# Optimization experiments

Hardware: AMD Instinct MI355X
Metric: run time of the kernel (lower is better)

The kernel has to match this reference:

```python
import jax, jax.numpy as jnp
import numpy as np
import math

N, D, H, DK, DV, FF = 2048, 1024, 16, 64, 64, 4096
EPS = 1e-5


def setup_inputs() -> dict:
    key = jax.random.key(0)
    ks = jax.random.split(key, 10)
    s = 0.02  # scaled init for numerical stability (original uses torch.randn)
    return {
        "x": jax.random.normal(ks[0], (N, D), dtype=jnp.float32),
        # per-head projections stacked: [H, D, DK/DV]
        "w_q": jax.random.normal(ks[1], (H, D, DK), dtype=jnp.float32) * s,
        "w_k": jax.random.normal(ks[2], (H, D, DK), dtype=jnp.float32) * s,
        "w_v": jax.random.normal(ks[3], (H, D, DV), dtype=jnp.float32) * s,
        "w_o": jax.random.normal(ks[4], (H * DV, D), dtype=jnp.float32) * s,
        "ln1_g": jnp.ones((D,), jnp.float32),
        "ln1_b": jnp.zeros((D,), jnp.float32),
        # FFN: Linear stored as [in, out] so y = x @ w + b
        "w1": jax.random.normal(ks[5], (D, FF), dtype=jnp.float32) * s,
        "b1": jnp.zeros((FF,), jnp.float32),
        "w2": jax.random.normal(ks[6], (FF, D), dtype=jnp.float32) * s,
        "b2": jnp.zeros((D,), jnp.float32),
        "ln2_g": jnp.ones((D,), jnp.float32),
        "ln2_b": jnp.zeros((D,), jnp.float32),
    }


def _layernorm(x, g, b):
    mu = jnp.mean(x, axis=-1, keepdims=True)
    var = jnp.mean(jnp.square(x - mu), axis=-1, keepdims=True)
    return (x - mu) * jax.lax.rsqrt(var + EPS) * g + b


def reference(x, w_q, w_k, w_v, w_o, ln1_g, ln1_b, w1, b1, w2, b2, ln2_g, ln2_b):
    n = x.shape[0]
    # multi-head causal self-attention (heads batched instead of Python loop)
    q = jnp.einsum('nd,hdk->hnk', x, w_q)  # [H,N,DK]
    k = jnp.einsum('nd,hdk->hnk', x, w_k)
    v = jnp.einsum('nd,hdv->hnv', x, w_v)
    scores = jnp.einsum('hnk,hmk->hnm', q, k) / math.sqrt(DK)  # [H,N,N]
    causal = jnp.tril(jnp.ones((n, n), dtype=bool))
    scores = jnp.where(causal, scores, -jnp.inf)
    probs = jax.nn.softmax(scores, axis=-1)
    attn = jnp.einsum('hnm,hmv->hnv', probs, v)  # [H,N,DV]
    concat = jnp.transpose(attn, (1, 0, 2)).reshape(n, H * DV)  # head-order concat
    mha = concat @ w_o  # [N,D]
    # residual + LN, FFN (note: ReLU after BOTH linears, as in the source)
    h = _layernorm(x + mha, ln1_g, ln1_b)
    ff = jax.nn.relu(jax.nn.relu(h @ w1 + b1) @ w2 + b2)
    return _layernorm(h + ff, ln2_g, ln2_b)
```

## Files before the change

### kernel.cpp

```cpp
#include <hip/hip_runtime.h>
#include <math.h>


#define NTOK   2048
#define DMODEL 1024
#define NHEAD  16
#define DHEAD  64
#define DFF    4096
#define LNEPS  1e-5f

typedef unsigned int   u32;
typedef unsigned short u16;
typedef __attribute__((ext_vector_type(8))) short short8;
typedef __attribute__((ext_vector_type(4))) float f32x4;

__device__ __forceinline__ u16 f2b(float f) {
    u32 b = __float_as_uint(f);
    b += 0x7FFFu + ((b >> 16) & 1u);
    return (u16)(b >> 16);
}

#define AS1(p) ((const __attribute__((address_space(1))) u32*)(p))
#define AS3(p) ((__attribute__((address_space(3))) u32*)(p))

template<int RELU, int BIAS, int RESID, int OUT_BF16, int SPLITK>
__global__ __launch_bounds__(256) void mfma_gemm(
    const u16* __restrict__ A, int lda,
    const u16* __restrict__ Bt, int ldbt,
    void* __restrict__ Cp, int ldc, int Kc,
    const float* __restrict__ bias,
    const float* __restrict__ resid, int ldr,
    size_t pstride)
{
    __shared__ u16 As[2][128 * 32];
    __shared__ u16 Bs[2][128 * 32];

    const int tid = threadIdx.x;
    const int l = tid & 63, w = tid >> 6;
    const int row0 = blockIdx.y * 128, col0 = blockIdx.x * 128;
    const int kbase = (SPLITK > 1) ? blockIdx.z * Kc : 0;

    f32x4 acc[4][4];
    #pragma unroll
    for (int m = 0; m < 4; ++m)
        #pragma unroll
        for (int n = 0; n < 4; ++n)
            acc[m][n] = (f32x4){0.f, 0.f, 0.f, 0.f};

    const int srow = w * 32 + (l >> 2);
    const int skk  = (l & 3) * 8;
    const u16* Ag = A  + (size_t)(row0 + srow) * lda  + kbase + skk;
    const u16* Bg = Bt + (size_t)(col0 + srow) * ldbt + kbase + skk;

    const int fr  = l & 15;
    const int fk  = (l >> 4) * 8;
    const int ar0 = (w >> 1) * 64;
    const int bc0 = (w & 1) * 64;

    auto STAGE = [&](int buf, int k0) {
        char* AsB = (char*)&As[buf][0] + w * 2048;
        char* BsB = (char*)&Bs[buf][0] + w * 2048;
        __builtin_amdgcn_global_load_lds(AS1(Ag + k0),                     AS3(AsB),        16, 0, 0);
        __builtin_amdgcn_global_load_lds(AS1(Ag + k0 + (size_t)16 * lda),  AS3(AsB + 1024), 16, 0, 0);
        __builtin_amdgcn_global_load_lds(AS1(Bg + k0),                     AS3(BsB),        16, 0, 0);
        __builtin_amdgcn_global_load_lds(AS1(Bg + k0 + (size_t)16 * ldbt), AS3(BsB + 1024), 16, 0, 0);
    };

    STAGE(0, 0);
    int cur = 0;
    for (int k0 = 0; k0 < Kc; k0 += 32) {
        __syncthreads();
        if (k0 + 32 < Kc) STAGE(cur ^ 1, k0 + 32);

        short8 af[4], bfr[4];
        #pragma unroll
        for (int m = 0; m < 4; ++m)
            af[m] = *reinterpret_cast<const short8*>(&As[cur][(ar0 + m * 16 + fr) * 32 + fk]);
        #pragma unroll
        for (int n = 0; n < 4; ++n)
            bfr[n] = *reinterpret_cast<const short8*>(&Bs[cur][(bc0 + n * 16 + fr) * 32 + fk]);
        #pragma unroll
        for (int m = 0; m < 4; ++m)
            #pragma unroll
            for (int n = 0; n < 4; ++n)
                acc[m][n] = __builtin_amdgcn_mfma_f32_16x16x32_bf16(af[m], bfr[n], acc[m][n], 0, 0, 0);
        cur ^= 1;
    }

    if (SPLITK > 1) {
        float* Pp = (float*)Cp + blockIdx.z * pstride;
        #pragma unroll
        for (int m = 0; m < 4; ++m)
            #pragma unroll
            for (int n = 0; n < 4; ++n)
                #pragma unroll
                for (int r = 0; r < 4; ++r) {
                    int row = row0 + ar0 + m * 16 + (l >> 4) * 4 + r;
                    int col = col0 + bc0 + n * 16 + (l & 15);
                    Pp[(size_t)row * ldc + col] = acc[m][n][r];
                }
        return;
    }

    #pragma unroll
    for (int m = 0; m < 4; ++m) {
        #pragma unroll
        for (int n = 0; n < 4; ++n) {
            #pragma unroll
            for (int r = 0; r < 4; ++r) {
                int row = row0 + ar0 + m * 16 + (l >> 4) * 4 + r;
                int col = col0 + bc0 + n * 16 + (l & 15);
                float val = acc[m][n][r];
                if (BIAS)  val += bias[col];
                if (RESID) val += resid[(size_t)row * ldr + col];
                if (RELU)  val = fmaxf(val, 0.0f);
                if (OUT_BF16) ((u16*)Cp)[(size_t)row * ldc + col] = f2b(val);
                else          ((float*)Cp)[(size_t)row * ldc + col] = val;
            }
        }
    }
}

__device__ __forceinline__ void transpose_tile32(
    const float* __restrict__ in, int ldin,
    u16* __restrict__ out, int ldout, int r0, int c0)
{
    __shared__ float tile[32][33];
    int tx = threadIdx.x & 31, ty = threadIdx.x >> 5;
    #pragma unroll
    for (int i = 0; i < 4; ++i) {
        int r = ty + i * 8;
        tile[r][tx] = in[(size_t)(r0 + r) * ldin + c0 + tx];
    }
    __syncthreads();
    #pragma unroll
    for (int i = 0; i < 4; ++i) {
        int rr = ty + i * 8;
        out[(size_t)(c0 + rr) * ldout + r0 + tx] = f2b(tile[tx][rr]);
    }
}

__global__ __launch_bounds__(256) void prep_all(
    const float* __restrict__ x,
    const float* __restrict__ wq, const float* __restrict__ wk, const float* __restrict__ wv,
    const float* __restrict__ wo, const float* __restrict__ w1, const float* __restrict__ w2,
    u16* __restrict__ xb, u16* __restrict__ wqkvT, u16* __restrict__ woT,
    u16* __restrict__ w1T, u16* __restrict__ w2T)
{
    int b = blockIdx.x;
    if (b < 1024) {
        int i = (b * 256 + threadIdx.x) * 8;
        float4 v0 = *reinterpret_cast<const float4*>(x + i);
        float4 v1 = *reinterpret_cast<const float4*>(x + i + 4);
        ushort4 o0, o1;
        o0.x = f2b(v0.x); o0.y = f2b(v0.y); o0.z = f2b(v0.z); o0.w = f2b(v0.w);
        o1.x = f2b(v1.x); o1.y = f2b(v1.y); o1.z = f2b(v1.z); o1.w = f2b(v1.w);
        *reinterpret_cast<ushort4*>(xb + i)     = o0;
        *reinterpret_cast<ushort4*>(xb + i + 4) = o1;
    } else if (b < 4096) {
        int u = b - 1024;
        int z = u >> 6, t = u & 63;
        int p = z >> 4, hh = z & 15;
        const float* in = (p == 0 ? wq : p == 1 ? wk : wv) + (size_t)hh * DMODEL * DHEAD;
        u16* out = wqkvT + (size_t)(p * 1024 + hh * 64) * DMODEL;
        transpose_tile32(in, DHEAD, out, DMODEL, (t >> 1) * 32, (t & 1) * 32);
    } else if (b < 5120) {
        int u = b - 4096;
        transpose_tile32(wo, DMODEL, woT, DMODEL, (u >> 5) * 32, (u & 31) * 32);
    } else if (b < 9216) {
        int u = b - 5120;
        transpose_tile32(w1, DFF, w1T, DMODEL, (u >> 7) * 32, (u & 127) * 32);
    } else {
        int u = b - 9216;
        transpose_tile32(w2, DMODEL, w2T, DFF, (u >> 5) * 32, (u & 31) * 32);
    }
}

__global__ __launch_bounds__(512) void flash_attn_mfma(
    const u16* __restrict__ qkvb, u16* __restrict__ concatb)
{
    const int bid = blockIdx.x;
    const int lo = bid & 255;
    int it = lo >> 3;
    int h  = lo & 7;
    if (bid >= 256) { it = 31 - it; h += 8; }

    const u16* qh = qkvb + h * DHEAD;
    const u16* kh = qkvb + DMODEL + h * DHEAD;
    const u16* vh = qkvb + 2 * DMODEL + h * DHEAD;
    const int LDQ = 3 * DMODEL;

    __shared__ u16 Ks[4][64][72];
    __shared__ u16 Vt[4][64][72];

    const int tid = threadIdx.x;
    const int l = tid & 63, w = tid >> 6;
    const int grp = w >> 2, wq = w & 3;
    const int fr = l & 15, fg = l >> 4;

    short8 qf[2];
    {
        const u16* qp = qh + (size_t)(it * 64 + wq * 16 + fr) * LDQ + fg * 8;
        qf[0] = *reinterpret_cast<const short8*>(qp);
        qf[1] = *reinterpret_cast<const short8*>(qp + 32);
    }

    const int kr  = tid >> 1;
    const int kb  = kr >> 6, krl = kr & 63;
    const int kc  = (tid & 1) * 32;
    const int vp  = tid >> 2;
    const int vb  = vp >> 5, vpl = vp & 31;
    const int vc  = (tid & 3) * 16;

    short8 kf[4], vf0[2], vf1[2];
    auto PREFETCH = [&](int s) {
        const u16* kg = kh + (size_t)(s * 256 + kr) * LDQ + kc;
        kf[0] = *reinterpret_cast<const short8*>(kg);
        kf[1] = *reinterpret_cast<const short8*>(kg + 8);
        kf[2] = *reinterpret_cast<const short8*>(kg + 16);
        kf[3] = *reinterpret_cast<const short8*>(kg + 24);
        const u16* vg = vh + (size_t)(s * 256 + 2 * vp) * LDQ + vc;
        vf0[0] = *reinterpret_cast<const short8*>(vg);
        vf0[1] = *reinterpret_cast<const short8*>(vg + 8);
        vf1[0] = *reinterpret_cast<const short8*>(vg + LDQ);
        vf1[1] = *reinterpret_cast<const short8*>(vg + LDQ + 8);
    };

    f32x4 o[4];
    #pragma unroll
    for (int n = 0; n < 4; ++n) o[n] = (f32x4){0.f, 0.f, 0.f, 0.f};
    float m_run = -INFINITY, l_run = 0.0f;

    const int sA = fr + 16 * ((2 * fg) & 3);
    const int sB = sA + 16;
    const bool hi = (fg >= 2);

    char* VtSb = (char*)&Vt[vb][0][0];

    const int niter = (it >> 2) + 1;
    PREFETCH(0);

    for (int s = 0; s < niter; ++s) {
        __syncthreads();
        *reinterpret_cast<short8*>(&Ks[kb][krl][kc +  0]) = kf[0];
        *reinterpret_cast<short8*>(&Ks[kb][krl][kc +  8]) = kf[1];
        *reinterpret_cast<short8*>(&Ks[kb][krl][kc + 16]) = kf[2];
        *reinterpret_cast<short8*>(&Ks[kb][krl][kc + 24]) = kf[3];
        #pragma unroll
        for (int c2 = 0; c2 < 2; ++c2) {
            #pragma unroll
            for (int i = 0; i < 8; ++i) {
                u32 word = (u32)(u16)vf0[c2][i] | ((u32)(u16)vf1[c2][i] << 16);
                int dv = vc + c2 * 8 + i;
                int off = 144 * dv + 16 * ((vpl >> 2) ^ ((dv >> 3) & 7)) + 4 * (vpl & 3);
                *reinterpret_cast<u32*>(VtSb + off) = word;
            }
        }
        if (s + 1 < niter) PREFETCH(s + 1);
        __syncthreads();

        #pragma unroll
        for (int t = 0; t < 2; ++t) {
            const int jt = 4 * s + 2 * grp + t;
            if (jt > it) continue;
            const int buf = 2 * grp + t;
            const u16 (*KsG)[72] = Ks[buf];
            char* VtG = (char*)&Vt[buf][0][0];

            f32x4 s_[4];
            #pragma unroll
            for (int n = 0; n < 4; ++n) s_[n] = (f32x4){0.f, 0.f, 0.f, 0.f};
            __builtin_amdgcn_s_setprio(1);
            #pragma unroll
            for (int n = 0; n < 4; ++n) {
                #pragma unroll
                for (int ks = 0; ks < 2; ++ks) {
                    short8 kfrag = *reinterpret_cast<const short8*>(&KsG[n * 16 + fr][ks * 32 + fg * 8]);
                    s_[n] = __builtin_amdgcn_mfma_f32_16x16x32_bf16(kfrag, qf[ks], s_[n], 0, 0, 0);
                }
            }
            __builtin_amdgcn_s_setprio(0);

            const bool diag = (jt == it);
            const int qrow_t = wq * 16 + fr;
            float sv[4][4];
            float pm = -INFINITY;
            #pragma unroll
            for (int n = 0; n < 4; ++n)
                #pragma unroll
                for (int r = 0; r < 4; ++r) {
                    float v = s_[n][r] * 0.125f;
                    if (diag && (n * 16 + fg * 4 + r) > qrow_t) v = -INFINITY;
                    sv[n][r] = v;
                    pm = fmaxf(pm, v);
                }
            pm = fmaxf(pm, __shfl_xor(pm, 16));
            pm = fmaxf(pm, __shfl_xor(pm, 32));
            if (!__all(pm <= m_run + 8.0f)) {
                float mnew = fmaxf(m_run, pm);
                float corr = __expf(m_run - mnew);
                l_run *= corr;
                #pragma unroll
                for (int n = 0; n < 4; ++n) {
                    o[n][0] *= corr; o[n][1] *= corr; o[n][2] *= corr; o[n][3] *= corr;
                }
                m_run = mnew;
            }
            float rs = 0.0f;
            float pp[4][4];
            #pragma unroll
            for (int n = 0; n < 4; ++n)
                #pragma unroll
                for (int r = 0; r < 4; ++r) {
                    float pv = __expf(sv[n][r] - m_run);
                    pp[n][r] = pv;
                    rs += pv;
                }
            rs += __shfl_xor(rs, 16);
            rs += __shfl_xor(rs, 32);
            l_run += rs;

            u32 pk[4][2];
            #pragma unroll
            for (int n = 0; n < 4; ++n) {
                pk[n][0] = (__float_as_uint(pp[n][0]) >> 16) | (__float_as_uint(pp[n][1]) & 0xFFFF0000u);
                pk[n][1] = (__float_as_uint(pp[n][2]) >> 16) | (__float_as_uint(pp[n][3]) & 0xFFFF0000u);
            }

            __builtin_amdgcn_s_setprio(1);
            #pragma unroll
            for (int ks = 0; ks < 2; ++ks) {
                u32 a0 = __shfl(pk[2 * ks][0], sA);
                u32 a1 = __shfl(pk[2 * ks][1], sA);
                u32 a2 = __shfl(pk[2 * ks][0], sB);
                u32 a3 = __shfl(pk[2 * ks][1], sB);
                u32 b0 = __shfl(pk[2 * ks + 1][0], sA);
                u32 b1 = __shfl(pk[2 * ks + 1][1], sA);
                u32 b2 = __shfl(pk[2 * ks + 1][0], sB);
                u32 b3 = __shfl(pk[2 * ks + 1][1], sB);
                union { u32 u[4]; short8 s8; } pb;
                pb.u[0] = hi ? b0 : a0;
                pb.u[1] = hi ? b1 : a1;
                pb.u[2] = hi ? b2 : a2;
                pb.u[3] = hi ? b3 : a3;
                #pragma unroll
                for (int n = 0; n < 4; ++n) {
                    int dv = n * 16 + fr;
                    const short8* vfrag = reinterpret_cast<const short8*>(
                        VtG + 144 * dv + 16 * ((ks * 4 + fg) ^ ((dv >> 3) & 7)));
                    o[n] = __builtin_amdgcn_mfma_f32_16x16x32_bf16(*vfrag, pb.s8, o[n], 0, 0, 0);
                }
            }
            __builtin_amdgcn_s_setprio(0);
        }
    }

    __syncthreads();
    float* mrg = reinterpret_cast<float*>(&Ks[0][0][0]);
    const int slot = (wq * 64 + l) * 18;
    if (grp == 1) {
        #pragma unroll
        for (int n = 0; n < 4; ++n)
            #pragma unroll
            for (int r = 0; r < 4; ++r)
                mrg[slot + n * 4 + r] = o[n][r];
        mrg[slot + 16] = m_run;
        mrg[slot + 17] = l_run;
    }
    __syncthreads();
    if (grp == 0) {
        float mB = mrg[slot + 16], lB = mrg[slot + 17];
        float mstar = fmaxf(m_run, mB);
        float cA = __expf(m_run - mstar);
        float cB = __expf(mB - mstar);
        float inv = 1.0f / (l_run * cA + lB * cB);
        int qrow = it * 64 + wq * 16 + fr;
        #pragma unroll
        for (int n = 0; n < 4; ++n)
            #pragma unroll
            for (int r = 0; r < 4; ++r) {
                float val = (o[n][r] * cA + mrg[slot + n * 4 + r] * cB) * inv;
                concatb[(size_t)qrow * DMODEL + h * DHEAD + n * 16 + fg * 4 + r] = f2b(val);
            }
    }
}

template<int NPART, int RELUB, int DUAL>
__global__ __launch_bounds__(256) void ln_fuse(
    const float* __restrict__ P, size_t pstride,
    const float* __restrict__ base,
    const float* __restrict__ bias2,
    const float* __restrict__ g, const float* __restrict__ b,
    float* __restrict__ out, u16* __restrict__ outb)
{
    int row = blockIdx.x, tid = threadIdx.x;
    __shared__ float red[256];
    size_t off = (size_t)row * DMODEL + tid * 4;

    float4 acc = *reinterpret_cast<const float4*>(P + off);
    #pragma unroll
    for (int p = 1; p < NPART; ++p) {
        float4 t = *reinterpret_cast<const float4*>(P + (size_t)p * pstride + off);
        acc.x += t.x; acc.y += t.y; acc.z += t.z; acc.w += t.w;
    }
    if (RELUB) {
        float4 bb = *reinterpret_cast<const float4*>(bias2 + tid * 4);
        acc.x = fmaxf(acc.x + bb.x, 0.0f); acc.y = fmaxf(acc.y + bb.y, 0.0f);
        acc.z = fmaxf(acc.z + bb.z, 0.0f); acc.w = fmaxf(acc.w + bb.w, 0.0f);
    }
    float4 bs = *reinterpret_cast<const float4*>(base + off);
    float vals[4] = {acc.x + bs.x, acc.y + bs.y, acc.z + bs.z, acc.w + bs.w};

    float s = vals[0] + vals[1] + vals[2] + vals[3];
    red[tid] = s; __syncthreads();
    for (int st = 128; st > 0; st >>= 1) { if (tid < st) red[tid] += red[tid + st]; __syncthreads(); }
    float mu = red[0] * (1.0f / DMODEL);
    __syncthreads();

    float vs = 0.0f;
    #pragma unroll
    for (int i = 0; i < 4; ++i) { float d = vals[i] - mu; vs += d * d; }
    red[tid] = vs; __syncthreads();
    for (int st = 128; st > 0; st >>= 1) { if (tid < st) red[tid] += red[tid + st]; __syncthreads(); }
    float rstd = rsqrtf(red[0] * (1.0f / DMODEL) + LNEPS);

    float4 gv = *reinterpret_cast<const float4*>(g + tid * 4);
    float4 bv = *reinterpret_cast<const float4*>(b + tid * 4);
    float gs[4] = {gv.x, gv.y, gv.z, gv.w};
    float bsc[4] = {bv.x, bv.y, bv.z, bv.w};
    #pragma unroll
    for (int i = 0; i < 4; ++i) {
        float r = (vals[i] - mu) * rstd * gs[i] + bsc[i];
        out[off + i] = r;
        if (DUAL) outb[off + i] = f2b(r);
    }
}

extern "C" void kernel_launch(void* const* d_in, const int* in_sizes, int n_in,
                              void* d_out, int out_size, void* d_ws, size_t ws_size,
                              hipStream_t stream)
{
    const float* x    = (const float*)d_in[0];
    const float* wq   = (const float*)d_in[1];
    const float* wk   = (const float*)d_in[2];
    const float* wv   = (const float*)d_in[3];
    const float* wo   = (const float*)d_in[4];
    const float* ln1g = (const float*)d_in[5];
    const float* ln1b = (const float*)d_in[6];
    const float* w1   = (const float*)d_in[7];
    const float* b1   = (const float*)d_in[8];
    const float* w2   = (const float*)d_in[9];
    const float* b2   = (const float*)d_in[10];
    const float* ln2g = (const float*)d_in[11];
    const float* ln2b = (const float*)d_in[12];
    float* out = (float*)d_out;

    char* ws = (char*)d_ws;
    const size_t MB = 1024 * 1024;
    u16*   w2T     = (u16*)  (ws + 0 * MB);
    float* h1      = (float*)(ws + 8 * MB);
    float* P01     = (float*)(ws + 16 * MB);
    u16*   ff1b    = (u16*)  (ws + 16 * MB);
    float* FP      = (float*)(ws + 32 * MB);
    u16*   wqkvT   = (u16*)  (ws + 32 * MB);
    u16*   woT     = (u16*)  (ws + 38 * MB);
    u16*   w1T     = (u16*)  (ws + 40 * MB);
    u16*   xb      = (u16*)  (ws + 48 * MB);
    u16*   concatb = (u16*)  (ws + 48 * MB);
    u16*   h1b     = (u16*)  (ws + 48 * MB);
    u16*   qkvb    = (u16*)  (ws + 52 * MB);

    const size_t PSTRIDE = (size_t)NTOK * DMODEL;

    dim3 blk(256);

    prep_all<<<dim3(13312), blk, 0, stream>>>(x, wq, wk, wv, wo, w1, w2,
                                              xb, wqkvT, woT, w1T, w2T);

    mfma_gemm<0,0,0,1,1><<<dim3(24, 16), blk, 0, stream>>>(
        xb, DMODEL, wqkvT, DMODEL, qkvb, 3 * DMODEL, DMODEL, nullptr, nullptr, 0, 0);
    flash_attn_mfma<<<dim3(512), dim3(512), 0, stream>>>(qkvb, concatb);
    mfma_gemm<0,0,0,0,2><<<dim3(8, 16, 2), blk, 0, stream>>>(
        concatb, DMODEL, woT, DMODEL, P01, DMODEL, 512, nullptr, nullptr, 0, PSTRIDE);
    ln_fuse<2,0,1><<<dim3(NTOK), blk, 0, stream>>>(
        P01, PSTRIDE, x, nullptr, ln1g, ln1b, h1, h1b);
    mfma_gemm<1,1,0,1,1><<<dim3(32, 16), blk, 0, stream>>>(
        h1b, DMODEL, w1T, DMODEL, ff1b, DFF, DMODEL, b1, nullptr, 0, 0);
    mfma_gemm<0,0,0,0,4><<<dim3(8, 16, 4), blk, 0, stream>>>(
        ff1b, DFF, w2T, DFF, FP, DMODEL, 1024, nullptr, nullptr, 0, PSTRIDE);
    ln_fuse<4,1,0><<<dim3(NTOK), blk, 0, stream>>>(
        FP, PSTRIDE, h1, b2, ln2g, ln2b, out, nullptr);
}
```

Baseline: 166.6 us.

## Store split-K partials in fp16, use bf16 residual, split out-proj 4 ways

Split-K partial sums are now written as fp16 instead of fp32, which halves the partial-buffer traffic in the GEMM epilogues and in the layernorm reductions. The fp32 h1 buffer is dropped: the second layernorm reads the bf16 copy h1b as its residual base. The output projection now uses 4-way split-K instead of 2-way, and the workspace layout is reorganised to match. The cost is lower precision: fp16 partials can overflow or lose precision, and the bf16 residual adds rounding error to the final output.

```diff
diff --git a/kernel.cpp b/kernel.cpp
--- a/kernel.cpp
+++ b/kernel.cpp
@@ -11,13 +11,18 @@
 
 typedef unsigned int   u32;
 typedef unsigned short u16;
+typedef _Float16       f16;
 typedef __attribute__((ext_vector_type(8))) short short8;
 typedef __attribute__((ext_vector_type(4))) float f32x4;
+typedef __attribute__((ext_vector_type(4))) _Float16 f16x4;
 
 __device__ __forceinline__ u16 f2b(float f) {
     u32 b = __float_as_uint(f);
     b += 0x7FFFu + ((b >> 16) & 1u);
     return (u16)(b >> 16);
+}
+__device__ __forceinline__ float b2f(u16 v) {
+    return __uint_as_float((u32)v << 16);
 }
 
 #define AS1(p) ((const __attribute__((address_space(1))) u32*)(p))
@@ -88,7 +93,7 @@
     }
 
     if (SPLITK > 1) {
-        float* Pp = (float*)Cp + blockIdx.z * pstride;
+        f16* Pp = (f16*)Cp + blockIdx.z * pstride;
         #pragma unroll
         for (int m = 0; m < 4; ++m)
             #pragma unroll
@@ -97,7 +102,7 @@
                 for (int r = 0; r < 4; ++r) {
                     int row = row0 + ar0 + m * 16 + (l >> 4) * 4 + r;
                     int col = col0 + bc0 + n * 16 + (l & 15);
-                    Pp[(size_t)row * ldc + col] = acc[m][n][r];
+                    Pp[(size_t)row * ldc + col] = (f16)acc[m][n][r];
                 }
         return;
     }
@@ -385,10 +390,10 @@
     }
 }
 
-template<int NPART, int RELUB, int DUAL>
+template<int NPART, int RELUB, int OUTF, int DUAL, int BASEBF16>
 __global__ __launch_bounds__(256) void ln_fuse(
-    const float* __restrict__ P, size_t pstride,
-    const float* __restrict__ base,
+    const f16* __restrict__ P, size_t pstride,
+    const void* __restrict__ basev,
     const float* __restrict__ bias2,
     const float* __restrict__ g, const float* __restrict__ b,
     float* __restrict__ out, u16* __restrict__ outb)
@@ -397,19 +402,26 @@
     __shared__ float red[256];
     size_t off = (size_t)row * DMODEL + tid * 4;
 
-    float4 acc = *reinterpret_cast<const float4*>(P + off);
-    #pragma unroll
-    for (int p = 1; p < NPART; ++p) {
-        float4 t = *reinterpret_cast<const float4*>(P + (size_t)p * pstride + off);
-        acc.x += t.x; acc.y += t.y; acc.z += t.z; acc.w += t.w;
+    float a0 = 0.f, a1 = 0.f, a2 = 0.f, a3 = 0.f;
+    #pragma unroll
+    for (int p = 0; p < NPART; ++p) {
+        f16x4 t = *reinterpret_cast<const f16x4*>(P + (size_t)p * pstride + off);
+        a0 += (float)t.x; a1 += (float)t.y; a2 += (float)t.z; a3 += (float)t.w;
     }
     if (RELUB) {
         float4 bb = *reinterpret_cast<const float4*>(bias2 + tid * 4);
-        acc.x = fmaxf(acc.x + bb.x, 0.0f); acc.y = fmaxf(acc.y + bb.y, 0.0f);
-        acc.z = fmaxf(acc.z + bb.z, 0.0f); acc.w = fmaxf(acc.w + bb.w, 0.0f);
-    }
-    float4 bs = *reinterpret_cast<const float4*>(base + off);
-    float vals[4] = {acc.x + bs.x, acc.y + bs.y, acc.z + bs.z, acc.w + bs.w};
+        a0 = fmaxf(a0 + bb.x, 0.0f); a1 = fmaxf(a1 + bb.y, 0.0f);
+        a2 = fmaxf(a2 + bb.z, 0.0f); a3 = fmaxf(a3 + bb.w, 0.0f);
+    }
+    float vals[4];
+    if (BASEBF16) {
+        ushort4 bs = *reinterpret_cast<const ushort4*>((const u16*)basev + off);
+        vals[0] = a0 + b2f(bs.x); vals[1] = a1 + b2f(bs.y);
+        vals[2] = a2 + b2f(bs.z); vals[3] = a3 + b2f(bs.w);
+    } else {
+        float4 bs = *reinterpret_cast<const float4*>((const float*)basev + off);
+        vals[0] = a0 + bs.x; vals[1] = a1 + bs.y; vals[2] = a2 + bs.z; vals[3] = a3 + bs.w;
+    }
 
     float s = vals[0] + vals[1] + vals[2] + vals[3];
     red[tid] = s; __syncthreads();
@@ -431,7 +443,7 @@
     #pragma unroll
     for (int i = 0; i < 4; ++i) {
         float r = (vals[i] - mu) * rstd * gs[i] + bsc[i];
-        out[off + i] = r;
+        if (OUTF) out[off + i] = r;
         if (DUAL) outb[off + i] = f2b(r);
     }
 }
@@ -457,18 +469,17 @@
 
     char* ws = (char*)d_ws;
     const size_t MB = 1024 * 1024;
-    u16*   w2T     = (u16*)  (ws + 0 * MB);
-    float* h1      = (float*)(ws + 8 * MB);
-    float* P01     = (float*)(ws + 16 * MB);
-    u16*   ff1b    = (u16*)  (ws + 16 * MB);
-    float* FP      = (float*)(ws + 32 * MB);
-    u16*   wqkvT   = (u16*)  (ws + 32 * MB);
-    u16*   woT     = (u16*)  (ws + 38 * MB);
-    u16*   w1T     = (u16*)  (ws + 40 * MB);
-    u16*   xb      = (u16*)  (ws + 48 * MB);
-    u16*   concatb = (u16*)  (ws + 48 * MB);
-    u16*   h1b     = (u16*)  (ws + 48 * MB);
-    u16*   qkvb    = (u16*)  (ws + 52 * MB);
+    u16* w2T     = (u16*)(ws + 0 * MB);
+    u16* w1T     = (u16*)(ws + 8 * MB);
+    u16* woT     = (u16*)(ws + 16 * MB);
+    u16* wqkvT   = (u16*)(ws + 18 * MB);
+    u16* xb      = (u16*)(ws + 24 * MB);
+    u16* ff1b    = (u16*)(ws + 24 * MB);
+    u16* qkvb    = (u16*)(ws + 28 * MB);
+    u16* concatb = (u16*)(ws + 40 * MB);
+    f16* Ph      = (f16*)(ws + 44 * MB);
+    f16* Fh      = (f16*)(ws + 44 * MB);
+    u16* h1b     = (u16*)(ws + 60 * MB);
 
     const size_t PSTRIDE = (size_t)NTOK * DMODEL;
 
@@ -480,14 +491,14 @@
     mfma_gemm<0,0,0,1,1><<<dim3(24, 16), blk, 0, stream>>>(
         xb, DMODEL, wqkvT, DMODEL, qkvb, 3 * DMODEL, DMODEL, nullptr, nullptr, 0, 0);
     flash_attn_mfma<<<dim3(512), dim3(512), 0, stream>>>(qkvb, concatb);
-    mfma_gemm<0,0,0,0,2><<<dim3(8, 16, 2), blk, 0, stream>>>(
-        concatb, DMODEL, woT, DMODEL, P01, DMODEL, 512, nullptr, nullptr, 0, PSTRIDE);
-    ln_fuse<2,0,1><<<dim3(NTOK), blk, 0, stream>>>(
-        P01, PSTRIDE, x, nullptr, ln1g, ln1b, h1, h1b);
+    mfma_gemm<0,0,0,0,4><<<dim3(8, 16, 4), blk, 0, stream>>>(
+        concatb, DMODEL, woT, DMODEL, Ph, DMODEL, 256, nullptr, nullptr, 0, PSTRIDE);
+    ln_fuse<4,0,0,1,0><<<dim3(NTOK), blk, 0, stream>>>(
+        Ph, PSTRIDE, x, nullptr, ln1g, ln1b, nullptr, h1b);
     mfma_gemm<1,1,0,1,1><<<dim3(32, 16), blk, 0, stream>>>(
         h1b, DMODEL, w1T, DMODEL, ff1b, DFF, DMODEL, b1, nullptr, 0, 0);
     mfma_gemm<0,0,0,0,4><<<dim3(8, 16, 4), blk, 0, stream>>>(
-        ff1b, DFF, w2T, DFF, FP, DMODEL, 1024, nullptr, nullptr, 0, PSTRIDE);
-    ln_fuse<4,1,0><<<dim3(NTOK), blk, 0, stream>>>(
-        FP, PSTRIDE, h1, b2, ln2g, ln2b, out, nullptr);
-}
+        ff1b, DFF, w2T, DFF, Fh, DMODEL, 1024, nullptr, nullptr, 0, PSTRIDE);
+    ln_fuse<4,1,1,0,1><<<dim3(NTOK), blk, 0, stream>>>(
+        Fh, PSTRIDE, h1b, b2, ln2g, ln2b, out, nullptr);
+}
```

Result: faster. 160.3 us (-3.8%).
